# Kernel optimization log

Measured on AMD Instinct MI355X. Metric: run time of the kernel, lower is better.

## Reference

```python
import jax, jax.numpy as jnp
import numpy as np
from jax import lax

B, T_HIST, T_PRED = 8192, 11, 80
IN, H = 2, 64


def _glorot(key, shape, fan):
    bound = 1.0 / np.sqrt(fan)
    return jax.random.uniform(key, shape, jnp.float32, -bound, bound)


def setup_inputs() -> dict:
    key = jax.random.key(0)
    ks = jax.random.split(key, 20)
    inp = {"x": jax.random.normal(ks[0], (B, T_HIST, IN), jnp.float32)}
    # encoder / decoder: 2-layer tanh RNN, PyTorch param layout (out_features first)
    for pfx, base in (("enc", 1), ("dec", 9)):
        inp[f"{pfx}_Wih0"] = _glorot(ks[base + 0], (H, IN), H)
        inp[f"{pfx}_Whh0"] = _glorot(ks[base + 1], (H, H), H)
        inp[f"{pfx}_bih0"] = _glorot(ks[base + 2], (H,), H)
        inp[f"{pfx}_bhh0"] = _glorot(ks[base + 3], (H,), H)
        inp[f"{pfx}_Wih1"] = _glorot(ks[base + 4], (H, H), H)
        inp[f"{pfx}_Whh1"] = _glorot(ks[base + 5], (H, H), H)
        inp[f"{pfx}_bih1"] = _glorot(ks[base + 6], (H,), H)
        inp[f"{pfx}_bhh1"] = _glorot(ks[base + 7], (H,), H)
    inp["fc_W"] = _glorot(ks[17], (2, H), H)
    inp["fc_b"] = _glorot(ks[18], (2,), H)
    return inp


def _rnn_layer(x_seq, h0, Wih, Whh, bih, bhh):
    # x_seq: [T, B, in]; tanh RNN cell, returns (h_T, all hidden states [T, B, H])
    def step(h, x_t):
        h_new = jnp.tanh(x_t @ Wih.T + bih + h @ Whh.T + bhh)
        return h_new, h_new
    return lax.scan(step, h0, x_seq)


def reference(x,
              enc_Wih0, enc_Whh0, enc_bih0, enc_bhh0,
              enc_Wih1, enc_Whh1, enc_bih1, enc_bhh1,
              dec_Wih0, dec_Whh0, dec_bih0, dec_bhh0,
              dec_Wih1, dec_Whh1, dec_bih1, dec_bhh1,
              fc_W, fc_b):
    b = x.shape[0]
    h0 = jnp.zeros((b, H), x.dtype)
    x_seq = jnp.swapaxes(x, 0, 1)  # [T, B, 2]
    # encoder (dropout inactive in eval)
    h1_T, hs0 = _rnn_layer(x_seq, h0, enc_Wih0, enc_Whh0, enc_bih0, enc_bhh0)
    h2_T, _ = _rnn_layer(hs0, h0, enc_Wih1, enc_Whh1, enc_bih1, enc_bhh1)

    def dec_step(carry, _):
        h1, h2, inp = carry
        h1 = jnp.tanh(inp @ dec_Wih0.T + dec_bih0 + h1 @ dec_Whh0.T + dec_bhh0)
        h2 = jnp.tanh(h1 @ dec_Wih1.T + dec_bih1 + h2 @ dec_Whh1.T + dec_bhh1)
        pred = h2 @ fc_W.T + fc_b  # [B, 2]
        return (h1, h2, pred), pred

    init = (h1_T, h2_T, x[:, -1, :])
    _, preds = lax.scan(dec_step, init, None, length=T_PRED)  # [80, B, 2]
    return jnp.swapaxes(preds, 0, 1)  # [B, 80, 2]
```

## Files before the change

kernel.cpp:

```cpp
#include <hip/hip_runtime.h>

typedef __attribute__((ext_vector_type(8))) _Float16 f16x8;
typedef __attribute__((ext_vector_type(4))) float   f32x4;

namespace {
constexpr int kB    = 8192;
constexpr int kTH   = 11;
constexpr int kTP   = 80;
constexpr int kM    = 16;
constexpr int kStrH = 72;
}

__device__ __forceinline__ f16x8 cvt8(const float* f) {
    f16x8 v;
#pragma unroll
    for (int j = 0; j < 8; ++j) v[j] = (_Float16)f[j];
    return v;
}

__device__ __forceinline__ void loadB1(const float* __restrict__ W, int col, int q,
                                       f16x8 (&Bf)[2]) {
#pragma unroll
    for (int c = 0; c < 2; ++c) {
        const float* src = W + col * 64 + c * 32 + q * 8;
        const float4 a = reinterpret_cast<const float4*>(src)[0];
        const float4 b = reinterpret_cast<const float4*>(src)[1];
        float f[8] = {a.x, a.y, a.z, a.w, b.x, b.y, b.z, b.w};
        Bf[c] = cvt8(f);
    }
}

__device__ __forceinline__ void loadBfc(const float* __restrict__ fcW, int p, int q,
                                        f16x8 (&Bf)[2]) {
#pragma unroll
    for (int c = 0; c < 2; ++c) {
        float f[8];
#pragma unroll
        for (int j = 0; j < 8; ++j)
            f[j] = (p < 2) ? fcW[p * 64 + c * 32 + q * 8 + j] : 0.f;
        Bf[c] = cvt8(f);
    }
}

__device__ __forceinline__ void loadBG(const float* __restrict__ fcW, float w0, float w1,
                                       int q, f16x8 (&Bf)[2]) {
#pragma unroll
    for (int c = 0; c < 2; ++c) {
        float f[8];
#pragma unroll
        for (int j = 0; j < 8; ++j) {
            const int k = c * 32 + q * 8 + j;
            f[j] = w0 * fcW[k] + w1 * fcW[64 + k];
        }
        Bf[c] = cvt8(f);
    }
}

__device__ __forceinline__ f16x8 read_frag(const _Float16* plane, int off) {
    return *reinterpret_cast<const f16x8*>(plane + off);
}

__device__ __forceinline__ f32x4 mfma1(f16x8 a, f16x8 b, f32x4 acc) {
    return __builtin_amdgcn_mfma_f32_16x16x32_f16(a, b, acc, 0, 0, 0);
}

__device__ __forceinline__ float fast_tanh(float x) {
    const float e = __builtin_amdgcn_exp2f(x * 2.8853900817779268f);
    return fmaf(-2.0f, __builtin_amdgcn_rcpf(e + 1.0f), 1.0f);
}

__global__ __attribute__((amdgpu_waves_per_eu(2, 2))) __launch_bounds__(256)
void traj_rnn_kernel(
    const float* __restrict__ x,
    const float* __restrict__ eWih0, const float* __restrict__ eWhh0,
    const float* __restrict__ ebih0, const float* __restrict__ ebhh0,
    const float* __restrict__ eWih1, const float* __restrict__ eWhh1,
    const float* __restrict__ ebih1, const float* __restrict__ ebhh1,
    const float* __restrict__ dWih0, const float* __restrict__ dWhh0,
    const float* __restrict__ dbih0, const float* __restrict__ dbhh0,
    const float* __restrict__ dWih1, const float* __restrict__ dWhh1,
    const float* __restrict__ dbih1, const float* __restrict__ dbhh1,
    const float* __restrict__ fcW, const float* __restrict__ fcb,
    float* __restrict__ out)
{
    const int tid  = threadIdx.x;
    const int wv   = tid >> 6;
    const int lane = tid & 63;
    const int p    = lane & 15;
    const int q    = lane >> 4;
    const int col  = wv * 16 + p;
    const int r0   = blockIdx.x * kM;

    __shared__ __align__(16) _Float16 Hhi1[kM * kStrH];
    __shared__ __align__(16) _Float16 Hhi2[kM * kStrH];
    __shared__ __align__(16) float xbuf[kM * kTH * 2];
    __shared__ __align__(16) float predbuf[kM * kTP * 2];

    for (int i = tid; i < kM * kTH * 2; i += 256)
        xbuf[i] = x[r0 * (kTH * 2) + i];

    f16x8 H1f[2], H2f[2];
#pragma unroll
    for (int c = 0; c < 2; ++c) {
        H1f[c] = f16x8{0, 0, 0, 0, 0, 0, 0, 0};
        H2f[c] = f16x8{0, 0, 0, 0, 0, 0, 0, 0};
    }
    __syncthreads();

    const int aoff = p * kStrH;

    {
        const float b0 = ebih0[col] + ebhh0[col];
        const float b1 = ebih1[col] + ebhh1[col];
        const float w0 = eWih0[col * 2 + 0];
        const float w1 = eWih0[col * 2 + 1];
        f16x8 B0[2], B1[2], B2[2];
        loadB1(eWhh0, col, q, B0);
        loadB1(eWih1, col, q, B1);
        loadB1(eWhh1, col, q, B2);

        f32x4 P1 = {b0, b0, b0, b0};

#pragma unroll 1
        for (int t = 0; t < kTH; ++t) {
#pragma unroll
            for (int r = 0; r < 4; ++r) {
                const float2 xv = *reinterpret_cast<const float2*>(
                    &xbuf[(4 * q + r) * (kTH * 2) + 2 * t]);
                const float h1 = fast_tanh(fmaf(w0, xv.x, fmaf(w1, xv.y, P1[r])));
                Hhi1[(4 * q + r) * kStrH + col] = (_Float16)h1;
            }
            f32x4 a2 = {b1, b1, b1, b1};
#pragma unroll
            for (int c = 0; c < 2; ++c)
                a2 = mfma1(H2f[c], B2[c], a2);
            __syncthreads();

#pragma unroll
            for (int c = 0; c < 2; ++c)
                H1f[c] = read_frag(Hhi1, aoff + c * 32 + q * 8);
#pragma unroll
            for (int c = 0; c < 2; ++c)
                a2 = mfma1(H1f[c], B1[c], a2);
#pragma unroll
            for (int r = 0; r < 4; ++r) {
                const float h2 = fast_tanh(a2[r]);
                Hhi2[(4 * q + r) * kStrH + col] = (_Float16)h2;
            }
            __syncthreads();

#pragma unroll
            for (int c = 0; c < 2; ++c)
                H2f[c] = read_frag(Hhi2, aoff + c * 32 + q * 8);
            f32x4 np = {b0, b0, b0, b0};
#pragma unroll
            for (int c = 0; c < 2; ++c)
                np = mfma1(H1f[c], B0[c], np);
            P1 = np;
        }
    }

    {
        const float b0 = dbih0[col] + dbhh0[col];
        const float b1 = dbih1[col] + dbhh1[col];
        const float w0 = dWih0[col * 2 + 0];
        const float w1 = dWih0[col * 2 + 1];
        const float fb0 = fcb[0];
        const float fb1 = fcb[1];
        const float b0p = b0 + w0 * fb0 + w1 * fb1;
        const float fbp = (p == 0) ? fb0 : fb1;
        f16x8 B0[2], B1[2], B2[2], BF[2], BG[2];
        loadB1(dWhh0, col, q, B0);
        loadB1(dWih1, col, q, B1);
        loadB1(dWhh1, col, q, B2);
        loadBfc(fcW, p, q, BF);
        loadBG(fcW, w0, w1, q, BG);

        f32x4 P1 = {b0, b0, b0, b0};
#pragma unroll
        for (int c = 0; c < 2; ++c)
            P1 = mfma1(H1f[c], B0[c], P1);
#pragma unroll
        for (int r = 0; r < 4; ++r) {
            const float2 xv = *reinterpret_cast<const float2*>(
                &xbuf[(4 * q + r) * (kTH * 2) + 2 * (kTH - 1)]);
            P1[r] = fmaf(w0, xv.x, fmaf(w1, xv.y, P1[r]));
        }

#pragma unroll 2
        for (int t = 0; t < kTP; ++t) {
#pragma unroll
            for (int r = 0; r < 4; ++r) {
                const float h1 = fast_tanh(P1[r]);
                Hhi1[(4 * q + r) * kStrH + col] = (_Float16)h1;
            }
            f32x4 a2 = {b1, b1, b1, b1};
#pragma unroll
            for (int c = 0; c < 2; ++c)
                a2 = mfma1(H2f[c], B2[c], a2);
            __syncthreads();

#pragma unroll
            for (int c = 0; c < 2; ++c)
                H1f[c] = read_frag(Hhi1, aoff + c * 32 + q * 8);
#pragma unroll
            for (int c = 0; c < 2; ++c)
                a2 = mfma1(H1f[c], B1[c], a2);
#pragma unroll
            for (int r = 0; r < 4; ++r) {
                const float h2 = fast_tanh(a2[r]);
                Hhi2[(4 * q + r) * kStrH + col] = (_Float16)h2;
            }
            __syncthreads();

#pragma unroll
            for (int c = 0; c < 2; ++c)
                H2f[c] = read_frag(Hhi2, aoff + c * 32 + q * 8);
            f32x4 ng = {b0p, b0p, b0p, b0p};
            f32x4 nb = {0.f, 0.f, 0.f, 0.f};
#pragma unroll
            for (int c = 0; c < 2; ++c) {
                ng = mfma1(H2f[c], BG[c], ng);
                nb = mfma1(H1f[c], B0[c], nb);
            }
            P1 = ng + nb;

            f32x4 fcC = {0.f, 0.f, 0.f, 0.f};
#pragma unroll
            for (int c = 0; c < 2; ++c)
                fcC = mfma1(H2f[c], BF[c], fcC);
            if (wv == 0 && p < 2) {
#pragma unroll
                for (int r = 0; r < 4; ++r)
                    predbuf[((4 * q + r) * kTP + t) * 2 + p] = fcC[r] + fbp;
            }
        }
    }

    __syncthreads();
    {
        float4* dst = reinterpret_cast<float4*>(out + r0 * (kTP * 2));
        const float4* src = reinterpret_cast<const float4*>(predbuf);
        for (int i = tid; i < kM * kTP * 2 / 4; i += 256)
            dst[i] = src[i];
    }
}

extern "C" void kernel_launch(void* const* d_in, const int* in_sizes, int n_in,
                              void* d_out, int out_size, void* d_ws, size_t ws_size,
                              hipStream_t stream) {
    const float* x     = (const float*)d_in[0];
    const float* eWih0 = (const float*)d_in[1];
    const float* eWhh0 = (const float*)d_in[2];
    const float* ebih0 = (const float*)d_in[3];
    const float* ebhh0 = (const float*)d_in[4];
    const float* eWih1 = (const float*)d_in[5];
    const float* eWhh1 = (const float*)d_in[6];
    const float* ebih1 = (const float*)d_in[7];
    const float* ebhh1 = (const float*)d_in[8];
    const float* dWih0 = (const float*)d_in[9];
    const float* dWhh0 = (const float*)d_in[10];
    const float* dbih0 = (const float*)d_in[11];
    const float* dbhh0 = (const float*)d_in[12];
    const float* dWih1 = (const float*)d_in[13];
    const float* dWhh1 = (const float*)d_in[14];
    const float* dbih1 = (const float*)d_in[15];
    const float* dbhh1 = (const float*)d_in[16];
    const float* fcW   = (const float*)d_in[17];
    const float* fcb   = (const float*)d_in[18];
    float* out = (float*)d_out;

    dim3 grid(kB / kM);
    dim3 block(256);
    traj_rnn_kernel<<<grid, block, 0, stream>>>(
        x, eWih0, eWhh0, ebih0, ebhh0, eWih1, eWhh1, ebih1, ebhh1,
        dWih0, dWhh0, dbih0, dbhh0, dWih1, dWhh1, dbih1, dbhh1,
        fcW, fcb, out);
}
```

Before: 141.0 us.

## Process two independent 16-row batch tiles per block to interleave MFMA chains

Each block now handles two independent groups of 16 batch rows, with separate LDS hidden-state buffers, and interleaves their MFMA and tanh sequences within each timestep. Independent work can then fill MFMA and LDS latency inside the serial recurrence, and the barriers per timestep are shared across twice as many rows. The cost is half as many blocks (256 for 8192 rows), more registers per thread and larger shared memory, so occupancy and the spread across CUs may drop. The decoder loop unroll also changes from 2 to 1.

```diff
diff --git a/kernel.cpp b/kernel.cpp
--- a/kernel.cpp
+++ b/kernel.cpp
@@ -9,6 +9,7 @@
 constexpr int kTP   = 80;
 constexpr int kM    = 16;
 constexpr int kStrH = 72;
+constexpr int kPB   = kM * kTP * 2;
 }
 
 __device__ __forceinline__ f16x8 cvt8(const float* f) {
@@ -89,26 +90,29 @@
     const int p    = lane & 15;
     const int q    = lane >> 4;
     const int col  = wv * 16 + p;
-    const int r0   = blockIdx.x * kM;
-
-    __shared__ __align__(16) _Float16 Hhi1[kM * kStrH];
-    __shared__ __align__(16) _Float16 Hhi2[kM * kStrH];
-    __shared__ __align__(16) float xbuf[kM * kTH * 2];
-    __shared__ __align__(16) float predbuf[kM * kTP * 2];
-
-    for (int i = tid; i < kM * kTH * 2; i += 256)
+    const int r0   = blockIdx.x * (2 * kM);
+
+    __shared__ __align__(16) _Float16 Hhi1a[kM * kStrH];
+    __shared__ __align__(16) _Float16 Hhi1b[kM * kStrH];
+    __shared__ __align__(16) _Float16 Hhi2a[kM * kStrH];
+    __shared__ __align__(16) _Float16 Hhi2b[kM * kStrH];
+    __shared__ __align__(16) float xbuf[2 * kM * kTH * 2];
+    __shared__ __align__(16) float predbuf[2 * kPB];
+
+    for (int i = tid; i < 2 * kM * kTH * 2; i += 256)
         xbuf[i] = x[r0 * (kTH * 2) + i];
 
-    f16x8 H1f[2], H2f[2];
-#pragma unroll
-    for (int c = 0; c < 2; ++c) {
-        H1f[c] = f16x8{0, 0, 0, 0, 0, 0, 0, 0};
-        H2f[c] = f16x8{0, 0, 0, 0, 0, 0, 0, 0};
-    }
+    const float* xbufA = xbuf;
+    const float* xbufB = xbuf + kM * kTH * 2;
+
+    const f16x8 Z = {0, 0, 0, 0, 0, 0, 0, 0};
+    f16x8 H1a0 = Z, H1a1 = Z, H1b0 = Z, H1b1 = Z;
+    f16x8 H2a0 = Z, H2a1 = Z, H2b0 = Z, H2b1 = Z;
     __syncthreads();
 
     const int aoff = p * kStrH;
 
+    f32x4 P1a, P1b;
     {
         const float b0 = ebih0[col] + ebhh0[col];
         const float b1 = ebih1[col] + ebhh1[col];
@@ -119,44 +123,55 @@
         loadB1(eWih1, col, q, B1);
         loadB1(eWhh1, col, q, B2);
 
-        f32x4 P1 = {b0, b0, b0, b0};
+        P1a = f32x4{b0, b0, b0, b0};
+        P1b = f32x4{b0, b0, b0, b0};
 
 #pragma unroll 1
         for (int t = 0; t < kTH; ++t) {
 #pragma unroll
             for (int r = 0; r < 4; ++r) {
                 const float2 xv = *reinterpret_cast<const float2*>(
-                    &xbuf[(4 * q + r) * (kTH * 2) + 2 * t]);
-                const float h1 = fast_tanh(fmaf(w0, xv.x, fmaf(w1, xv.y, P1[r])));
-                Hhi1[(4 * q + r) * kStrH + col] = (_Float16)h1;
+                    &xbufA[(4 * q + r) * (kTH * 2) + 2 * t]);
+                Hhi1a[(4 * q + r) * kStrH + col] =
+                    (_Float16)fast_tanh(fmaf(w0, xv.x, fmaf(w1, xv.y, P1a[r])));
             }
-            f32x4 a2 = {b1, b1, b1, b1};
-#pragma unroll
-            for (int c = 0; c < 2; ++c)
-                a2 = mfma1(H2f[c], B2[c], a2);
+#pragma unroll
+            for (int r = 0; r < 4; ++r) {
+                const float2 xv = *reinterpret_cast<const float2*>(
+                    &xbufB[(4 * q + r) * (kTH * 2) + 2 * t]);
+                Hhi1b[(4 * q + r) * kStrH + col] =
+                    (_Float16)fast_tanh(fmaf(w0, xv.x, fmaf(w1, xv.y, P1b[r])));
+            }
+            f32x4 a2a = {b1, b1, b1, b1};
+            f32x4 a2b = {b1, b1, b1, b1};
+            a2a = mfma1(H2a0, B2[0], a2a);  a2b = mfma1(H2b0, B2[0], a2b);
+            a2a = mfma1(H2a1, B2[1], a2a);  a2b = mfma1(H2b1, B2[1], a2b);
             __syncthreads();
 
-#pragma unroll
-            for (int c = 0; c < 2; ++c)
-                H1f[c] = read_frag(Hhi1, aoff + c * 32 + q * 8);
-#pragma unroll
-            for (int c = 0; c < 2; ++c)
-                a2 = mfma1(H1f[c], B1[c], a2);
-#pragma unroll
-            for (int r = 0; r < 4; ++r) {
-                const float h2 = fast_tanh(a2[r]);
-                Hhi2[(4 * q + r) * kStrH + col] = (_Float16)h2;
-            }
+            H1a0 = read_frag(Hhi1a, aoff + q * 8);
+            H1a1 = read_frag(Hhi1a, aoff + 32 + q * 8);
+            H1b0 = read_frag(Hhi1b, aoff + q * 8);
+            H1b1 = read_frag(Hhi1b, aoff + 32 + q * 8);
+            a2a = mfma1(H1a0, B1[0], a2a);  a2b = mfma1(H1b0, B1[0], a2b);
+            a2a = mfma1(H1a1, B1[1], a2a);  a2b = mfma1(H1b1, B1[1], a2b);
+#pragma unroll
+            for (int r = 0; r < 4; ++r)
+                Hhi2a[(4 * q + r) * kStrH + col] = (_Float16)fast_tanh(a2a[r]);
+#pragma unroll
+            for (int r = 0; r < 4; ++r)
+                Hhi2b[(4 * q + r) * kStrH + col] = (_Float16)fast_tanh(a2b[r]);
             __syncthreads();
 
-#pragma unroll
-            for (int c = 0; c < 2; ++c)
-                H2f[c] = read_frag(Hhi2, aoff + c * 32 + q * 8);
-            f32x4 np = {b0, b0, b0, b0};
-#pragma unroll
-            for (int c = 0; c < 2; ++c)
-                np = mfma1(H1f[c], B0[c], np);
-            P1 = np;
+            H2a0 = read_frag(Hhi2a, aoff + q * 8);
+            H2a1 = read_frag(Hhi2a, aoff + 32 + q * 8);
+            H2b0 = read_frag(Hhi2b, aoff + q * 8);
+            H2b1 = read_frag(Hhi2b, aoff + 32 + q * 8);
+            f32x4 npa = {b0, b0, b0, b0};
+            f32x4 npb = {b0, b0, b0, b0};
+            npa = mfma1(H1a0, B0[0], npa);  npb = mfma1(H1b0, B0[0], npb);
+            npa = mfma1(H1a1, B0[1], npa);  npb = mfma1(H1b1, B0[1], npb);
+            P1a = npa;
+            P1b = npb;
         }
     }
 
@@ -176,63 +191,79 @@
         loadBfc(fcW, p, q, BF);
         loadBG(fcW, w0, w1, q, BG);
 
-        f32x4 P1 = {b0, b0, b0, b0};
-#pragma unroll
-        for (int c = 0; c < 2; ++c)
-            P1 = mfma1(H1f[c], B0[c], P1);
+        P1a = f32x4{b0, b0, b0, b0};
+        P1b = f32x4{b0, b0, b0, b0};
+        P1a = mfma1(H1a0, B0[0], P1a);  P1b = mfma1(H1b0, B0[0], P1b);
+        P1a = mfma1(H1a1, B0[1], P1a);  P1b = mfma1(H1b1, B0[1], P1b);
 #pragma unroll
         for (int r = 0; r < 4; ++r) {
             const float2 xv = *reinterpret_cast<const float2*>(
-                &xbuf[(4 * q + r) * (kTH * 2) + 2 * (kTH - 1)]);
-            P1[r] = fmaf(w0, xv.x, fmaf(w1, xv.y, P1[r]));
-        }
-
-#pragma unroll 2
+                &xbufA[(4 * q + r) * (kTH * 2) + 2 * (kTH - 1)]);
+            P1a[r] = fmaf(w0, xv.x, fmaf(w1, xv.y, P1a[r]));
+        }
+#pragma unroll
+        for (int r = 0; r < 4; ++r) {
+            const float2 xv = *reinterpret_cast<const float2*>(
+                &xbufB[(4 * q + r) * (kTH * 2) + 2 * (kTH - 1)]);
+            P1b[r] = fmaf(w0, xv.x, fmaf(w1, xv.y, P1b[r]));
+        }
+
+#pragma unroll 1
         for (int t = 0; t < kTP; ++t) {
 #pragma unroll
-            for (int r = 0; r < 4; ++r) {
-                const float h1 = fast_tanh(P1[r]);
-                Hhi1[(4 * q + r) * kStrH + col] = (_Float16)h1;
+            for (int r = 0; r < 4; ++r)
+                Hhi1a[(4 * q + r) * kStrH + col] = (_Float16)fast_tanh(P1a[r]);
+#pragma unroll
+            for (int r = 0; r < 4; ++r)
+                Hhi1b[(4 * q + r) * kStrH + col] = (_Float16)fast_tanh(P1b[r]);
+            f32x4 a2a = {b1, b1, b1, b1};
+            f32x4 a2b = {b1, b1, b1, b1};
+            a2a = mfma1(H2a0, B2[0], a2a);  a2b = mfma1(H2b0, B2[0], a2b);
+            a2a = mfma1(H2a1, B2[1], a2a);  a2b = mfma1(H2b1, B2[1], a2b);
+            __syncthreads();
+
+            H1a0 = read_frag(Hhi1a, aoff + q * 8);
+            H1a1 = read_frag(Hhi1a, aoff + 32 + q * 8);
+            H1b0 = read_frag(Hhi1b, aoff + q * 8);
+            H1b1 = read_frag(Hhi1b, aoff + 32 + q * 8);
+            a2a = mfma1(H1a0, B1[0], a2a);  a2b = mfma1(H1b0, B1[0], a2b);
+            a2a = mfma1(H1a1, B1[1], a2a);  a2b = mfma1(H1b1, B1[1], a2b);
+#pragma unroll
+            for (int r = 0; r < 4; ++r)
+                Hhi2a[(4 * q + r) * kStrH + col] = (_Float16)fast_tanh(a2a[r]);
+#pragma unroll
+            for (int r = 0; r < 4; ++r)
+                Hhi2b[(4 * q + r) * kStrH + col] = (_Float16)fast_tanh(a2b[r]);
+            __syncthreads();
+
+            H2a0 = read_frag(Hhi2a, aoff + q * 8);
+            H2a1 = read_frag(Hhi2a, aoff + 32 + q * 8);
+            H2b0 = read_frag(Hhi2b, aoff + q * 8);
+            H2b1 = read_frag(Hhi2b, aoff + 32 + q * 8);
+            f32x4 nga = {b0p, b0p, b0p, b0p};
+            f32x4 ngb = {b0p, b0p, b0p, b0p};
+            f32x4 nba = {0.f, 0.f, 0.f, 0.f};
+            f32x4 nbb = {0.f, 0.f, 0.f, 0.f};
+            nga = mfma1(H2a0, BG[0], nga);  nba = mfma1(H1a0, B0[0], nba);
+            ngb = mfma1(H2b0, BG[0], ngb);  nbb = mfma1(H1b0, B0[0], nbb);
+            nga = mfma1(H2a1, BG[1], nga);  nba = mfma1(H1a1, B0[1], nba);
+            ngb = mfma1(H2b1, BG[1], ngb);  nbb = mfma1(H1b1, B0[1], nbb);
+            P1a = nga + nba;
+            P1b = ngb + nbb;
+
+            f32x4 fc0 = {0.f, 0.f, 0.f, 0.f};
+            f32x4 fc1 = {0.f, 0.f, 0.f, 0.f};
+            fc0 = mfma1(H2a0, BF[0], fc0);  fc1 = mfma1(H2b0, BF[0], fc1);
+            fc0 = mfma1(H2a1, BF[1], fc0);  fc1 = mfma1(H2b1, BF[1], fc1);
+            if (wv == 0 && p < 2) {
+#pragma unroll
+                for (int r = 0; r < 4; ++r)
+                    predbuf[((4 * q + r) * kTP + t) * 2 + p] = fc0[r] + fbp;
             }
-            f32x4 a2 = {b1, b1, b1, b1};
-#pragma unroll
-            for (int c = 0; c < 2; ++c)
-                a2 = mfma1(H2f[c], B2[c], a2);
-            __syncthreads();
-
-#pragma unroll
-            for (int c = 0; c < 2; ++c)
-                H1f[c] = read_frag(Hhi1, aoff + c * 32 + q * 8);
-#pragma unroll
-            for (int c = 0; c < 2; ++c)
-                a2 = mfma1(H1f[c], B1[c], a2);
-#pragma unroll
-            for (int r = 0; r < 4; ++r) {
-                const float h2 = fast_tanh(a2[r]);
-                Hhi2[(4 * q + r) * kStrH + col] = (_Float16)h2;
-            }
-            __syncthreads();
-
-#pragma unroll
-            for (int c = 0; c < 2; ++c)
-                H2f[c] = read_frag(Hhi2, aoff + c * 32 + q * 8);
-            f32x4 ng = {b0p, b0p, b0p, b0p};
-            f32x4 nb = {0.f, 0.f, 0.f, 0.f};
-#pragma unroll
-            for (int c = 0; c < 2; ++c) {
-                ng = mfma1(H2f[c], BG[c], ng);
-                nb = mfma1(H1f[c], B0[c], nb);
-            }
-            P1 = ng + nb;
-
-            f32x4 fcC = {0.f, 0.f, 0.f, 0.f};
-#pragma unroll
-            for (int c = 0; c < 2; ++c)
-                fcC = mfma1(H2f[c], BF[c], fcC);
-            if (wv == 0 && p < 2) {
+            if (wv == 1 && p < 2) {
 #pragma unroll
                 for (int r = 0; r < 4; ++r)
-                    predbuf[((4 * q + r) * kTP + t) * 2 + p] = fcC[r] + fbp;
+                    predbuf[kPB + ((4 * q + r) * kTP + t) * 2 + p] = fc1[r] + fbp;
             }
         }
     }
@@ -241,7 +272,7 @@
     {
         float4* dst = reinterpret_cast<float4*>(out + r0 * (kTP * 2));
         const float4* src = reinterpret_cast<const float4*>(predbuf);
-        for (int i = tid; i < kM * kTP * 2 / 4; i += 256)
+        for (int i = tid; i < 2 * kPB / 4; i += 256)
             dst[i] = src[i];
     }
 }
@@ -270,7 +301,7 @@
     const float* fcb   = (const float*)d_in[18];
     float* out = (float*)d_out;
 
-    dim3 grid(kB / kM);
+    dim3 grid(kB / (2 * kM));
     dim3 block(256);
     traj_rnn_kernel<<<grid, block, 0, stream>>>(
         x, eWih0, eWhh0, ebih0, ebhh0, eWih1, eWhh1, ebih1, ebhh1,
```

Result: slower. 159.2 us (+12.9%).

## Collapse each block to a single wave computing all hidden columns, dropping barriers

Applied to the files above, without the earlier changes.

Each workgroup now runs one 64-lane wave instead of four. That wave covers all 64 hidden columns by looping over four 16-column MFMA tiles, so the per-step __syncthreads on the recurrent state exchange are no longer needed. The intent is to remove barrier latency in the serial 91-step recurrence and let the MFMA chains from independent column tiles overlap. In exchange, register pressure goes up sharply (weight fragments grow from 2 to 8 per matrix), which may lower occupancy or cause spills. Each wave also does four times the serial work per step.

```diff
diff --git a/kernel.cpp b/kernel.cpp
--- a/kernel.cpp
+++ b/kernel.cpp
@@ -8,7 +8,7 @@
 constexpr int kTH   = 11;
 constexpr int kTP   = 80;
 constexpr int kM    = 16;
-constexpr int kStrH = 72;
+constexpr int kStr  = 72;
 }
 
 __device__ __forceinline__ f16x8 cvt8(const float* f) {
@@ -69,7 +69,7 @@
     return fmaf(-2.0f, __builtin_amdgcn_rcpf(e + 1.0f), 1.0f);
 }
 
-__global__ __attribute__((amdgpu_waves_per_eu(2, 2))) __launch_bounds__(256)
+__global__ __launch_bounds__(64)
 void traj_rnn_kernel(
     const float* __restrict__ x,
     const float* __restrict__ eWih0, const float* __restrict__ eWhh0,
@@ -83,43 +83,44 @@
     const float* __restrict__ fcW, const float* __restrict__ fcb,
     float* __restrict__ out)
 {
-    const int tid  = threadIdx.x;
-    const int wv   = tid >> 6;
-    const int lane = tid & 63;
+    const int lane = threadIdx.x;
     const int p    = lane & 15;
     const int q    = lane >> 4;
-    const int col  = wv * 16 + p;
     const int r0   = blockIdx.x * kM;
 
-    __shared__ __align__(16) _Float16 Hhi1[kM * kStrH];
-    __shared__ __align__(16) _Float16 Hhi2[kM * kStrH];
+    __shared__ __align__(16) _Float16 h1buf[kM * kStr];
+    __shared__ __align__(16) _Float16 h2buf[kM * kStr];
     __shared__ __align__(16) float xbuf[kM * kTH * 2];
     __shared__ __align__(16) float predbuf[kM * kTP * 2];
 
-    for (int i = tid; i < kM * kTH * 2; i += 256)
+    for (int i = lane; i < kM * kTH * 2; i += 64)
         xbuf[i] = x[r0 * (kTH * 2) + i];
 
-    f16x8 H1f[2], H2f[2];
-#pragma unroll
-    for (int c = 0; c < 2; ++c) {
-        H1f[c] = f16x8{0, 0, 0, 0, 0, 0, 0, 0};
-        H2f[c] = f16x8{0, 0, 0, 0, 0, 0, 0, 0};
-    }
-    __syncthreads();
-
-    const int aoff = p * kStrH;
+    const f16x8 Z = {0, 0, 0, 0, 0, 0, 0, 0};
+    f16x8 H1f[2] = {Z, Z};
+    f16x8 H2f[2] = {Z, Z};
+
+    const int aoff = p * kStr;
+
+    f32x4 P1[4];
 
     {
-        const float b0 = ebih0[col] + ebhh0[col];
-        const float b1 = ebih1[col] + ebhh1[col];
-        const float w0 = eWih0[col * 2 + 0];
-        const float w1 = eWih0[col * 2 + 1];
-        f16x8 B0[2], B1[2], B2[2];
-        loadB1(eWhh0, col, q, B0);
-        loadB1(eWih1, col, q, B1);
-        loadB1(eWhh1, col, q, B2);
-
-        f32x4 P1 = {b0, b0, b0, b0};
+        float b0[4], b1[4], w0[4], w1[4];
+        f16x8 B0[8], B1[8], B2[8];
+#pragma unroll
+        for (int n = 0; n < 4; ++n) {
+            const int col = p + 16 * n;
+            b0[n] = ebih0[col] + ebhh0[col];
+            b1[n] = ebih1[col] + ebhh1[col];
+            w0[n] = eWih0[col * 2 + 0];
+            w1[n] = eWih0[col * 2 + 1];
+            f16x8 t[2];
+            loadB1(eWhh0, col, q, t); B0[2 * n] = t[0]; B0[2 * n + 1] = t[1];
+            loadB1(eWih1, col, q, t); B1[2 * n] = t[0]; B1[2 * n + 1] = t[1];
+            loadB1(eWhh1, col, q, t); B2[2 * n] = t[0]; B2[2 * n + 1] = t[1];
+        }
+#pragma unroll
+        for (int n = 0; n < 4; ++n) P1[n] = f32x4{b0[n], b0[n], b0[n], b0[n]};
 
 #pragma unroll 1
         for (int t = 0; t < kTH; ++t) {
@@ -127,109 +128,135 @@
             for (int r = 0; r < 4; ++r) {
                 const float2 xv = *reinterpret_cast<const float2*>(
                     &xbuf[(4 * q + r) * (kTH * 2) + 2 * t]);
-                const float h1 = fast_tanh(fmaf(w0, xv.x, fmaf(w1, xv.y, P1[r])));
-                Hhi1[(4 * q + r) * kStrH + col] = (_Float16)h1;
+#pragma unroll
+                for (int n = 0; n < 4; ++n) {
+                    const float h1 = fast_tanh(fmaf(w0[n], xv.x, fmaf(w1[n], xv.y, P1[n][r])));
+                    h1buf[(4 * q + r) * kStr + p + 16 * n] = (_Float16)h1;
+                }
             }
-            f32x4 a2 = {b1, b1, b1, b1};
-#pragma unroll
-            for (int c = 0; c < 2; ++c)
-                a2 = mfma1(H2f[c], B2[c], a2);
-            __syncthreads();
-
-#pragma unroll
-            for (int c = 0; c < 2; ++c)
-                H1f[c] = read_frag(Hhi1, aoff + c * 32 + q * 8);
-#pragma unroll
-            for (int c = 0; c < 2; ++c)
-                a2 = mfma1(H1f[c], B1[c], a2);
-#pragma unroll
-            for (int r = 0; r < 4; ++r) {
-                const float h2 = fast_tanh(a2[r]);
-                Hhi2[(4 * q + r) * kStrH + col] = (_Float16)h2;
-            }
-            __syncthreads();
-
-#pragma unroll
-            for (int c = 0; c < 2; ++c)
-                H2f[c] = read_frag(Hhi2, aoff + c * 32 + q * 8);
-            f32x4 np = {b0, b0, b0, b0};
-#pragma unroll
-            for (int c = 0; c < 2; ++c)
-                np = mfma1(H1f[c], B0[c], np);
-            P1 = np;
+            f32x4 a2[4];
+#pragma unroll
+            for (int n = 0; n < 4; ++n) a2[n] = f32x4{b1[n], b1[n], b1[n], b1[n]};
+#pragma unroll
+            for (int c = 0; c < 2; ++c)
+#pragma unroll
+                for (int n = 0; n < 4; ++n)
+                    a2[n] = mfma1(H2f[c], B2[2 * n + c], a2[n]);
+            H1f[0] = read_frag(h1buf, aoff + q * 8);
+            H1f[1] = read_frag(h1buf, aoff + 32 + q * 8);
+#pragma unroll
+            for (int c = 0; c < 2; ++c)
+#pragma unroll
+                for (int n = 0; n < 4; ++n)
+                    a2[n] = mfma1(H1f[c], B1[2 * n + c], a2[n]);
+#pragma unroll
+            for (int n = 0; n < 4; ++n)
+#pragma unroll
+                for (int r = 0; r < 4; ++r)
+                    h2buf[(4 * q + r) * kStr + p + 16 * n] = (_Float16)fast_tanh(a2[n][r]);
+            f32x4 np[4];
+#pragma unroll
+            for (int n = 0; n < 4; ++n) np[n] = f32x4{b0[n], b0[n], b0[n], b0[n]};
+#pragma unroll
+            for (int c = 0; c < 2; ++c)
+#pragma unroll
+                for (int n = 0; n < 4; ++n)
+                    np[n] = mfma1(H1f[c], B0[2 * n + c], np[n]);
+            H2f[0] = read_frag(h2buf, aoff + q * 8);
+            H2f[1] = read_frag(h2buf, aoff + 32 + q * 8);
+#pragma unroll
+            for (int n = 0; n < 4; ++n) P1[n] = np[n];
         }
     }
 
     {
-        const float b0 = dbih0[col] + dbhh0[col];
-        const float b1 = dbih1[col] + dbhh1[col];
-        const float w0 = dWih0[col * 2 + 0];
-        const float w1 = dWih0[col * 2 + 1];
+        float b1[4], w0[4], w1[4], b0p[4];
+        f16x8 B0[8], B1[8], B2[8], BG[8], BF[2];
         const float fb0 = fcb[0];
         const float fb1 = fcb[1];
-        const float b0p = b0 + w0 * fb0 + w1 * fb1;
         const float fbp = (p == 0) ? fb0 : fb1;
-        f16x8 B0[2], B1[2], B2[2], BF[2], BG[2];
-        loadB1(dWhh0, col, q, B0);
-        loadB1(dWih1, col, q, B1);
-        loadB1(dWhh1, col, q, B2);
+        float b0[4];
+#pragma unroll
+        for (int n = 0; n < 4; ++n) {
+            const int col = p + 16 * n;
+            b0[n] = dbih0[col] + dbhh0[col];
+            b1[n] = dbih1[col] + dbhh1[col];
+            w0[n] = dWih0[col * 2 + 0];
+            w1[n] = dWih0[col * 2 + 1];
+            b0p[n] = b0[n] + w0[n] * fb0 + w1[n] * fb1;
+            f16x8 t[2];
+            loadB1(dWhh0, col, q, t); B0[2 * n] = t[0]; B0[2 * n + 1] = t[1];
+            loadB1(dWih1, col, q, t); B1[2 * n] = t[0]; B1[2 * n + 1] = t[1];
+            loadB1(dWhh1, col, q, t); B2[2 * n] = t[0]; B2[2 * n + 1] = t[1];
+            loadBG(fcW, w0[n], w1[n], q, t); BG[2 * n] = t[0]; BG[2 * n + 1] = t[1];
+        }
         loadBfc(fcW, p, q, BF);
-        loadBG(fcW, w0, w1, q, BG);
-
-        f32x4 P1 = {b0, b0, b0, b0};
+
+#pragma unroll
+        for (int n = 0; n < 4; ++n) P1[n] = f32x4{b0[n], b0[n], b0[n], b0[n]};
 #pragma unroll
         for (int c = 0; c < 2; ++c)
-            P1 = mfma1(H1f[c], B0[c], P1);
+#pragma unroll
+            for (int n = 0; n < 4; ++n)
+                P1[n] = mfma1(H1f[c], B0[2 * n + c], P1[n]);
 #pragma unroll
         for (int r = 0; r < 4; ++r) {
             const float2 xv = *reinterpret_cast<const float2*>(
                 &xbuf[(4 * q + r) * (kTH * 2) + 2 * (kTH - 1)]);
-            P1[r] = fmaf(w0, xv.x, fmaf(w1, xv.y, P1[r]));
-        }
-
-#pragma unroll 2
+#pragma unroll
+            for (int n = 0; n < 4; ++n)
+                P1[n][r] = fmaf(w0[n], xv.x, fmaf(w1[n], xv.y, P1[n][r]));
+        }
+
+#pragma unroll 1
         for (int t = 0; t < kTP; ++t) {
 #pragma unroll
-            for (int r = 0; r < 4; ++r) {
-                const float h1 = fast_tanh(P1[r]);
-                Hhi1[(4 * q + r) * kStrH + col] = (_Float16)h1;
+            for (int n = 0; n < 4; ++n)
+#pragma unroll
+                for (int r = 0; r < 4; ++r)
+                    h1buf[(4 * q + r) * kStr + p + 16 * n] = (_Float16)fast_tanh(P1[n][r]);
+            f32x4 a2[4];
+#pragma unroll
+            for (int n = 0; n < 4; ++n) a2[n] = f32x4{b1[n], b1[n], b1[n], b1[n]};
+#pragma unroll
+            for (int c = 0; c < 2; ++c)
+#pragma unroll
+                for (int n = 0; n < 4; ++n)
+                    a2[n] = mfma1(H2f[c], B2[2 * n + c], a2[n]);
+            H1f[0] = read_frag(h1buf, aoff + q * 8);
+            H1f[1] = read_frag(h1buf, aoff + 32 + q * 8);
+#pragma unroll
+            for (int c = 0; c < 2; ++c)
+#pragma unroll
+                for (int n = 0; n < 4; ++n)
+                    a2[n] = mfma1(H1f[c], B1[2 * n + c], a2[n]);
+#pragma unroll
+            for (int n = 0; n < 4; ++n)
+#pragma unroll
+                for (int r = 0; r < 4; ++r)
+                    h2buf[(4 * q + r) * kStr + p + 16 * n] = (_Float16)fast_tanh(a2[n][r]);
+            f32x4 nb[4];
+#pragma unroll
+            for (int n = 0; n < 4; ++n) nb[n] = f32x4{0.f, 0.f, 0.f, 0.f};
+#pragma unroll
+            for (int c = 0; c < 2; ++c)
+#pragma unroll
+                for (int n = 0; n < 4; ++n)
+                    nb[n] = mfma1(H1f[c], B0[2 * n + c], nb[n]);
+            H2f[0] = read_frag(h2buf, aoff + q * 8);
+            H2f[1] = read_frag(h2buf, aoff + 32 + q * 8);
+#pragma unroll
+            for (int n = 0; n < 4; ++n) {
+                f32x4 ng = f32x4{b0p[n], b0p[n], b0p[n], b0p[n]};
+#pragma unroll
+                for (int c = 0; c < 2; ++c)
+                    ng = mfma1(H2f[c], BG[2 * n + c], ng);
+                P1[n] = ng + nb[n];
             }
-            f32x4 a2 = {b1, b1, b1, b1};
-#pragma unroll
-            for (int c = 0; c < 2; ++c)
-                a2 = mfma1(H2f[c], B2[c], a2);
-            __syncthreads();
-
-#pragma unroll
-            for (int c = 0; c < 2; ++c)
-                H1f[c] = read_frag(Hhi1, aoff + c * 32 + q * 8);
-#pragma unroll
-            for (int c = 0; c < 2; ++c)
-                a2 = mfma1(H1f[c], B1[c], a2);
-#pragma unroll
-            for (int r = 0; r < 4; ++r) {
-                const float h2 = fast_tanh(a2[r]);
-                Hhi2[(4 * q + r) * kStrH + col] = (_Float16)h2;
-            }
-            __syncthreads();
-
-#pragma unroll
-            for (int c = 0; c < 2; ++c)
-                H2f[c] = read_frag(Hhi2, aoff + c * 32 + q * 8);
-            f32x4 ng = {b0p, b0p, b0p, b0p};
-            f32x4 nb = {0.f, 0.f, 0.f, 0.f};
-#pragma unroll
-            for (int c = 0; c < 2; ++c) {
-                ng = mfma1(H2f[c], BG[c], ng);
-                nb = mfma1(H1f[c], B0[c], nb);
-            }
-            P1 = ng + nb;
-
-            f32x4 fcC = {0.f, 0.f, 0.f, 0.f};
-#pragma unroll
-            for (int c = 0; c < 2; ++c)
-                fcC = mfma1(H2f[c], BF[c], fcC);
-            if (wv == 0 && p < 2) {
+            f32x4 fcC = f32x4{0.f, 0.f, 0.f, 0.f};
+            fcC = mfma1(H2f[0], BF[0], fcC);
+            fcC = mfma1(H2f[1], BF[1], fcC);
+            if (p < 2) {
 #pragma unroll
                 for (int r = 0; r < 4; ++r)
                     predbuf[((4 * q + r) * kTP + t) * 2 + p] = fcC[r] + fbp;
@@ -237,11 +264,11 @@
         }
     }
 
-    __syncthreads();
     {
         float4* dst = reinterpret_cast<float4*>(out + r0 * (kTP * 2));
         const float4* src = reinterpret_cast<const float4*>(predbuf);
-        for (int i = tid; i < kM * kTP * 2 / 4; i += 256)
+#pragma unroll 1
+        for (int i = lane; i < kM * kTP * 2 / 4; i += 64)
             dst[i] = src[i];
     }
 }
@@ -271,7 +298,7 @@
     float* out = (float*)d_out;
 
     dim3 grid(kB / kM);
-    dim3 block(256);
+    dim3 block(64);
     traj_rnn_kernel<<<grid, block, 0, stream>>>(
         x, eWih0, eWhh0, ebih0, ebhh0, eWih1, eWhh1, ebih1, ebhh1,
         dWih0, dWhh0, dbih0, dbhh0, dWih1, dWhh1, dbih1, dbhh1,
```

Result: slower. 191.7 us (+35.9%).

## Stagger blocks with sleep, raise priority on critical path, hoist H1 MFMA before barrier

Applied to the files above, without the earlier changes.

Half of the blocks, picked by an XOR hash of the block index, sleep briefly at startup so that co-resident blocks fall out of phase and their MFMA and barrier phases interleave. s_setprio raises wave priority around the serial-dependency work (tanh plus LDS stores, fragment reads, next-step MFMAs). The H1-dependent MFMA for the next step is moved ahead of the second barrier so it overlaps with barrier wait. The changes add scheduling hints and a small startup delay but do no extra arithmetic.

```diff
diff --git a/kernel.cpp b/kernel.cpp
--- a/kernel.cpp
+++ b/kernel.cpp
@@ -107,6 +107,11 @@
     }
     __syncthreads();
 
+    if ((blockIdx.x ^ (blockIdx.x >> 3) ^ (blockIdx.x >> 8)) & 1) {
+        __builtin_amdgcn_s_sleep(7);
+        __builtin_amdgcn_s_sleep(7);
+    }
+
     const int aoff = p * kStrH;
 
     {
@@ -123,6 +128,7 @@
 
 #pragma unroll 1
         for (int t = 0; t < kTH; ++t) {
+            __builtin_amdgcn_s_setprio(1);
 #pragma unroll
             for (int r = 0; r < 4; ++r) {
                 const float2 xv = *reinterpret_cast<const float2*>(
@@ -130,32 +136,32 @@
                 const float h1 = fast_tanh(fmaf(w0, xv.x, fmaf(w1, xv.y, P1[r])));
                 Hhi1[(4 * q + r) * kStrH + col] = (_Float16)h1;
             }
+            __builtin_amdgcn_s_setprio(0);
             f32x4 a2 = {b1, b1, b1, b1};
-#pragma unroll
-            for (int c = 0; c < 2; ++c)
-                a2 = mfma1(H2f[c], B2[c], a2);
-            __syncthreads();
-
-#pragma unroll
-            for (int c = 0; c < 2; ++c)
-                H1f[c] = read_frag(Hhi1, aoff + c * 32 + q * 8);
-#pragma unroll
-            for (int c = 0; c < 2; ++c)
-                a2 = mfma1(H1f[c], B1[c], a2);
+            a2 = mfma1(H2f[0], B2[0], a2);
+            a2 = mfma1(H2f[1], B2[1], a2);
+            __syncthreads();
+
+            __builtin_amdgcn_s_setprio(1);
+            H1f[0] = read_frag(Hhi1, aoff + q * 8);
+            H1f[1] = read_frag(Hhi1, aoff + 32 + q * 8);
+            a2 = mfma1(H1f[0], B1[0], a2);
+            a2 = mfma1(H1f[1], B1[1], a2);
 #pragma unroll
             for (int r = 0; r < 4; ++r) {
                 const float h2 = fast_tanh(a2[r]);
                 Hhi2[(4 * q + r) * kStrH + col] = (_Float16)h2;
             }
-            __syncthreads();
-
-#pragma unroll
-            for (int c = 0; c < 2; ++c)
-                H2f[c] = read_frag(Hhi2, aoff + c * 32 + q * 8);
+            __builtin_amdgcn_s_setprio(0);
             f32x4 np = {b0, b0, b0, b0};
-#pragma unroll
-            for (int c = 0; c < 2; ++c)
-                np = mfma1(H1f[c], B0[c], np);
+            np = mfma1(H1f[0], B0[0], np);
+            np = mfma1(H1f[1], B0[1], np);
+            __syncthreads();
+
+            __builtin_amdgcn_s_setprio(1);
+            H2f[0] = read_frag(Hhi2, aoff + q * 8);
+            H2f[1] = read_frag(Hhi2, aoff + 32 + q * 8);
+            __builtin_amdgcn_s_setprio(0);
             P1 = np;
         }
     }
@@ -177,9 +183,8 @@
         loadBG(fcW, w0, w1, q, BG);
 
         f32x4 P1 = {b0, b0, b0, b0};
-#pragma unroll
-        for (int c = 0; c < 2; ++c)
-            P1 = mfma1(H1f[c], B0[c], P1);
+        P1 = mfma1(H1f[0], B0[0], P1);
+        P1 = mfma1(H1f[1], B0[1], P1);
 #pragma unroll
         for (int r = 0; r < 4; ++r) {
             const float2 xv = *reinterpret_cast<const float2*>(
@@ -189,46 +194,46 @@
 
 #pragma unroll 2
         for (int t = 0; t < kTP; ++t) {
+            __builtin_amdgcn_s_setprio(1);
 #pragma unroll
             for (int r = 0; r < 4; ++r) {
                 const float h1 = fast_tanh(P1[r]);
                 Hhi1[(4 * q + r) * kStrH + col] = (_Float16)h1;
             }
+            __builtin_amdgcn_s_setprio(0);
             f32x4 a2 = {b1, b1, b1, b1};
-#pragma unroll
-            for (int c = 0; c < 2; ++c)
-                a2 = mfma1(H2f[c], B2[c], a2);
-            __syncthreads();
-
-#pragma unroll
-            for (int c = 0; c < 2; ++c)
-                H1f[c] = read_frag(Hhi1, aoff + c * 32 + q * 8);
-#pragma unroll
-            for (int c = 0; c < 2; ++c)
-                a2 = mfma1(H1f[c], B1[c], a2);
+            a2 = mfma1(H2f[0], B2[0], a2);
+            a2 = mfma1(H2f[1], B2[1], a2);
+            __syncthreads();
+
+            __builtin_amdgcn_s_setprio(1);
+            H1f[0] = read_frag(Hhi1, aoff + q * 8);
+            H1f[1] = read_frag(Hhi1, aoff + 32 + q * 8);
+            a2 = mfma1(H1f[0], B1[0], a2);
+            a2 = mfma1(H1f[1], B1[1], a2);
 #pragma unroll
             for (int r = 0; r < 4; ++r) {
                 const float h2 = fast_tanh(a2[r]);
                 Hhi2[(4 * q + r) * kStrH + col] = (_Float16)h2;
             }
-            __syncthreads();
-
-#pragma unroll
-            for (int c = 0; c < 2; ++c)
-                H2f[c] = read_frag(Hhi2, aoff + c * 32 + q * 8);
+            __builtin_amdgcn_s_setprio(0);
+            f32x4 nb = {0.f, 0.f, 0.f, 0.f};
+            nb = mfma1(H1f[0], B0[0], nb);
+            nb = mfma1(H1f[1], B0[1], nb);
+            __syncthreads();
+
+            __builtin_amdgcn_s_setprio(1);
+            H2f[0] = read_frag(Hhi2, aoff + q * 8);
+            H2f[1] = read_frag(Hhi2, aoff + 32 + q * 8);
             f32x4 ng = {b0p, b0p, b0p, b0p};
-            f32x4 nb = {0.f, 0.f, 0.f, 0.f};
-#pragma unroll
-            for (int c = 0; c < 2; ++c) {
-                ng = mfma1(H2f[c], BG[c], ng);
-                nb = mfma1(H1f[c], B0[c], nb);
-            }
+            ng = mfma1(H2f[0], BG[0], ng);
+            ng = mfma1(H2f[1], BG[1], ng);
             P1 = ng + nb;
+            __builtin_amdgcn_s_setprio(0);
 
             f32x4 fcC = {0.f, 0.f, 0.f, 0.f};
-#pragma unroll
-            for (int c = 0; c < 2; ++c)
-                fcC = mfma1(H2f[c], BF[c], fcC);
+            fcC = mfma1(H2f[0], BF[0], fcC);
+            fcC = mfma1(H2f[1], BF[1], fcC);
             if (wv == 0 && p < 2) {
 #pragma unroll
                 for (int r = 0; r < 4; ++r)
```

Result: slower. 144.9 us (+2.7%).
